# Kernel optimization log

Hardware: AMD Instinct MI355X
Metric: run time of the kernel (lower is better)

Reference implementation:

```python
import jax, jax.numpy as jnp
import numpy as np
from jax import lax

B, T, D = 2, 1024, 2048
HK, HV = 8, 16          # num key heads / num value heads
DK, DV = 128, 128       # head dims
KW = 4                  # conv kernel size
EPS = 1e-6
KEY_DIM = HK * DK
VALUE_DIM = HV * DV
CONV_DIM = 2 * KEY_DIM + VALUE_DIM


def setup_inputs() -> dict:
    key = jax.random.key(0)
    ks = jax.random.split(key, 9)
    w = lambda k, shape, s=0.02: jax.random.normal(k, shape, jnp.float32) * s
    return {
        'hidden_states': jax.random.normal(ks[0], (B, T, D), jnp.float32),
        'W_qkv': w(ks[1], (D, CONV_DIM)),
        'W_z': w(ks[2], (D, VALUE_DIM)),
        'W_b': w(ks[3], (D, HV)),
        'W_a': w(ks[4], (D, HV)),
        'conv_w': w(ks[5], (CONV_DIM, KW), 0.5),
        'dt_bias': jnp.ones((HV,), jnp.float32),
        'A_log': jnp.log(jax.random.uniform(ks[6], (HV,), jnp.float32, 1e-3, 16.0)),
        'norm_weight': jnp.ones((DV,), jnp.float32),
        'W_out': w(ks[7], (VALUE_DIM, D)),
    }


def _causal_conv_silu(x, w):
    # x: [B, C, T], w: [C, K] depthwise causal conv + SiLU (causal_conv1d_fn)
    k = w.shape[1]
    xp = jnp.pad(x, ((0, 0), (0, 0), (k - 1, 0)))
    y = sum(w[:, j][None, :, None] * xp[:, :, j:j + x.shape[2]] for j in range(k))
    return jax.nn.silu(y)


def _l2norm(x):
    return x * lax.rsqrt(jnp.sum(x * x, -1, keepdims=True) + 1e-6)


def reference(hidden_states, W_qkv, W_z, W_b, W_a, conv_w, dt_bias, A_log,
              norm_weight, W_out):
    Bb, Tt, _ = hidden_states.shape
    mixed = hidden_states @ W_qkv                       # [B,T,conv_dim]
    mixed = _causal_conv_silu(mixed.transpose(0, 2, 1), conv_w).transpose(0, 2, 1)
    q, k, v = jnp.split(mixed, [KEY_DIM, 2 * KEY_DIM], axis=-1)
    q = q.reshape(Bb, Tt, HK, DK)
    k = k.reshape(Bb, Tt, HK, DK)
    v = v.reshape(Bb, Tt, HV, DV)
    z = (hidden_states @ W_z).reshape(Bb, Tt, HV, DV)
    beta = jax.nn.sigmoid(hidden_states @ W_b)          # [B,T,HV]
    g = -jnp.exp(A_log) * jax.nn.softplus(hidden_states @ W_a + dt_bias)  # [B,T,HV]

    rep = HV // HK  # GQA: repeat_interleave q,k heads
    q = jnp.repeat(q, rep, axis=2)
    k = jnp.repeat(k, rep, axis=2)
    q = _l2norm(q) * (DK ** -0.5)                       # use_qk_l2norm + scale
    k = _l2norm(k)

    # gated delta-rule recurrence (fp32 state), scanned over time
    qs = q.transpose(1, 0, 2, 3)   # [T,B,HV,DK]
    ks = k.transpose(1, 0, 2, 3)
    vs = v.transpose(1, 0, 2, 3)   # [T,B,HV,DV]
    gs = g.transpose(1, 0, 2)      # [T,B,HV]
    bs = beta.transpose(1, 0, 2)

    def step(S, inp):
        qt, kt, vt, gt, bt = inp
        S = S * jnp.exp(gt)[..., None, None]                          # decay
        v_adj = (vt - jnp.einsum('bhk,bhkv->bhv', kt, S)) * bt[..., None]
        S = S + kt[..., None] * v_adj[..., None, :]                   # rank-1 delta update
        o = jnp.einsum('bhk,bhkv->bhv', qt, S)
        return S, o

    S0 = jnp.zeros((Bb, HV, DK, DV), jnp.float32)
    _, o = lax.scan(step, S0, (qs, ks, vs, gs, bs))
    o = o.transpose(1, 0, 2, 3)                         # [B,T,HV,DV]

    # gated RMSNorm over head_v_dim
    var = jnp.mean(o * o, -1, keepdims=True)
    o = o * lax.rsqrt(var + EPS) * norm_weight
    o = o * jax.nn.silu(z)

    return o.reshape(Bb, Tt, VALUE_DIM) @ W_out         # [B,T,D]
```

## Files before the change

### kernel.cpp

```cpp
#include <hip/hip_runtime.h>
#include <hip/hip_bf16.h>

#define B_ 2
#define T_ 1024
#define D_ 2048
#define HK_ 8
#define HV_ 16
#define DK_ 128
#define DV_ 128
#define KEY_DIM_ 1024
#define VALUE_DIM_ 2048
#define CONV_DIM_ 4096
#define BT_ 2048
#define NCH_ 16
#define CL_ 64

typedef __attribute__((ext_vector_type(8))) short short8;
typedef __attribute__((ext_vector_type(4))) float f32x4;

__device__ __forceinline__ short f2bf(float x) {
  __hip_bfloat16 h = __float2bfloat16(x);
  return *reinterpret_cast<short*>(&h);
}
__device__ __forceinline__ float bf2f(short u) {
  unsigned int x = ((unsigned int)(unsigned short)u) << 16;
  return __int_as_float(x);
}

#define GLOAD_LDS16(g, l)                                             \
  __builtin_amdgcn_global_load_lds(                                   \
      (const __attribute__((address_space(1))) void*)(g),             \
      (__attribute__((address_space(3))) void*)(l), 16, 0, 0)

__global__ void transpose_cast(const float* __restrict__ W, short* __restrict__ WT, int R, int C) {
  __shared__ float tile[32][33];
  int tx = threadIdx.x, ty = threadIdx.y;
  int x = blockIdx.x * 32 + tx;
#pragma unroll
  for (int j = 0; j < 4; ++j) {
    int r = blockIdx.y * 32 + ty + j * 8;
    tile[ty + j * 8][tx] = W[(long)r * C + x];
  }
  __syncthreads();
  int ro = blockIdx.y * 32 + tx;
#pragma unroll
  for (int j = 0; j < 4; ++j) {
    int co = blockIdx.x * 32 + ty + j * 8;
    WT[(long)co * R + ro] = f2bf(tile[tx][ty + j * 8]);
  }
}

__global__ void interleave_ba(const float* __restrict__ Wb, const float* __restrict__ Wa,
                              float* __restrict__ Wba32) {
  int i = blockIdx.x * 256 + threadIdx.x;
  int c = i & 31, k = i >> 5;
  Wba32[i] = (c < 16) ? Wb[k * 16 + c] : Wa[k * 16 + (c - 16)];
}

__global__ __launch_bounds__(256) void gemm128_split(const short* __restrict__ A,
                                                     const short* __restrict__ Bt,
                                                     float* __restrict__ C0,
                                                     float* __restrict__ C1,
                                                     int N0, int N1, int K) {
  __shared__ short As[2][128 * 32];
  __shared__ short Bs[2][128 * 32];
  int m0 = blockIdx.y * 128, n0 = blockIdx.x * 128;
  int tid = threadIdx.x;
  int wave = tid >> 6, lane = tid & 63;
  int wm = (wave >> 1) * 64, wn = (wave & 1) * 64;
  int quad = lane >> 4, l16 = lane & 15;
  f32x4 acc[4][4] = {};

  int ar = tid >> 2;
  int ac = (tid & 3) * 8;
  const short* Ag0 = A + (long)(m0 + ar) * K + ac;
  const short* Ag1 = A + (long)(m0 + 64 + ar) * K + ac;
  const short* Bg0 = Bt + (long)(n0 + ar) * K + ac;
  const short* Bg1 = Bt + (long)(n0 + 64 + ar) * K + ac;
  int NT = K >> 5;

#define STAGE_(t, c)                                  \
  do {                                                \
    GLOAD_LDS16(Ag0 + (t) * 32, As[c] + tid * 8);     \
    GLOAD_LDS16(Ag1 + (t) * 32, As[c] + 64 * 32 + tid * 8); \
    GLOAD_LDS16(Bg0 + (t) * 32, Bs[c] + tid * 8);     \
    GLOAD_LDS16(Bg1 + (t) * 32, Bs[c] + 64 * 32 + tid * 8); \
  } while (0)

  STAGE_(0, 0);
  STAGE_(1, 1);

  for (int t = 0; t < NT; ++t) {
    int c = t & 1;
    if (t + 1 < NT) {
      asm volatile("s_waitcnt vmcnt(4)" ::: "memory");
    } else {
      asm volatile("s_waitcnt vmcnt(0)" ::: "memory");
    }
    __builtin_amdgcn_s_barrier();
    __builtin_amdgcn_sched_barrier(0);

    short8 af[4], bf_[4];
#pragma unroll
    for (int i = 0; i < 4; ++i) af[i] = *(const short8*)(As[c] + (wm + i * 16 + l16) * 32 + quad * 8);
#pragma unroll
    for (int j = 0; j < 4; ++j) bf_[j] = *(const short8*)(Bs[c] + (wn + j * 16 + l16) * 32 + quad * 8);
#pragma unroll
    for (int i = 0; i < 4; ++i)
#pragma unroll
      for (int j = 0; j < 4; ++j)
        acc[i][j] = __builtin_amdgcn_mfma_f32_16x16x32_bf16(af[i], bf_[j], acc[i][j], 0, 0, 0);

    __builtin_amdgcn_sched_barrier(0);
    __builtin_amdgcn_s_barrier();
    if (t + 2 < NT) STAGE_(t + 2, c);
  }

  float* Cw; int ldc, cb;
  if (n0 < N0) { Cw = C0; ldc = N0; cb = n0; }
  else         { Cw = C1; ldc = N1; cb = n0 - N0; }
#pragma unroll
  for (int i = 0; i < 4; ++i)
#pragma unroll
    for (int j = 0; j < 4; ++j)
#pragma unroll
      for (int r = 0; r < 4; ++r) {
        int row = m0 + wm + i * 16 + quad * 4 + r;
        int colx = cb + wn + j * 16 + l16;
        Cw[(long)row * ldc + colx] = acc[i][j][r];
      }
#undef STAGE_
}

__global__ __launch_bounds__(256) void gemm128_ks(const short* __restrict__ A,
                                                  const short* __restrict__ Bt,
                                                  float* __restrict__ Cp,
                                                  int M, int N, int K) {
  __shared__ short As[2][128 * 32];
  __shared__ short Bs[2][128 * 32];
  int m0 = blockIdx.y * 128, n0 = blockIdx.x * 128;
  int kh = K >> 1;
  int kbeg = blockIdx.z * kh;
  int tid = threadIdx.x;
  int wave = tid >> 6, lane = tid & 63;
  int wm = (wave >> 1) * 64, wn = (wave & 1) * 64;
  int quad = lane >> 4, l16 = lane & 15;
  f32x4 acc[4][4] = {};

  int ar = tid >> 2;
  int ac = (tid & 3) * 8;
  const short* Ag0 = A + (long)(m0 + ar) * K + ac + kbeg;
  const short* Ag1 = A + (long)(m0 + 64 + ar) * K + ac + kbeg;
  const short* Bg0 = Bt + (long)(n0 + ar) * K + ac + kbeg;
  const short* Bg1 = Bt + (long)(n0 + 64 + ar) * K + ac + kbeg;
  int NT = kh >> 5;

#define STAGE_(t, c)                                  \
  do {                                                \
    GLOAD_LDS16(Ag0 + (t) * 32, As[c] + tid * 8);     \
    GLOAD_LDS16(Ag1 + (t) * 32, As[c] + 64 * 32 + tid * 8); \
    GLOAD_LDS16(Bg0 + (t) * 32, Bs[c] + tid * 8);     \
    GLOAD_LDS16(Bg1 + (t) * 32, Bs[c] + 64 * 32 + tid * 8); \
  } while (0)

  STAGE_(0, 0);
  STAGE_(1, 1);

  for (int t = 0; t < NT; ++t) {
    int c = t & 1;
    if (t + 1 < NT) {
      asm volatile("s_waitcnt vmcnt(4)" ::: "memory");
    } else {
      asm volatile("s_waitcnt vmcnt(0)" ::: "memory");
    }
    __builtin_amdgcn_s_barrier();
    __builtin_amdgcn_sched_barrier(0);

    short8 af[4], bf_[4];
#pragma unroll
    for (int i = 0; i < 4; ++i) af[i] = *(const short8*)(As[c] + (wm + i * 16 + l16) * 32 + quad * 8);
#pragma unroll
    for (int j = 0; j < 4; ++j) bf_[j] = *(const short8*)(Bs[c] + (wn + j * 16 + l16) * 32 + quad * 8);
#pragma unroll
    for (int i = 0; i < 4; ++i)
#pragma unroll
      for (int j = 0; j < 4; ++j)
        acc[i][j] = __builtin_amdgcn_mfma_f32_16x16x32_bf16(af[i], bf_[j], acc[i][j], 0, 0, 0);

    __builtin_amdgcn_sched_barrier(0);
    __builtin_amdgcn_s_barrier();
    if (t + 2 < NT) STAGE_(t + 2, c);
  }

  float* Cz = Cp + (long)blockIdx.z * M * N;
#pragma unroll
  for (int i = 0; i < 4; ++i)
#pragma unroll
    for (int j = 0; j < 4; ++j)
#pragma unroll
      for (int r = 0; r < 4; ++r) {
        int row = m0 + wm + i * 16 + quad * 4 + r;
        int colx = n0 + wn + j * 16 + l16;
        Cz[(long)row * N + colx] = acc[i][j][r];
      }
#undef STAGE_
}

__global__ void add2(const float* __restrict__ p0, const float* __restrict__ p1,
                     float* __restrict__ out, int n4) {
  int i = blockIdx.x * 256 + threadIdx.x;
  if (i < n4) {
    float4 a = ((const float4*)p0)[i];
    float4 b = ((const float4*)p1)[i];
    float4 o;
    o.x = a.x + b.x; o.y = a.y + b.y; o.z = a.z + b.z; o.w = a.w + b.w;
    ((float4*)out)[i] = o;
  }
}

__global__ __launch_bounds__(256) void small_proj(const float* __restrict__ hidden,
                                                  const float* __restrict__ Wba32,
                                                  const float* __restrict__ dt_bias,
                                                  const float* __restrict__ A_log,
                                                  float* __restrict__ betaT,
                                                  float* __restrict__ gT,
                                                  short* __restrict__ hbf) {
  __shared__ float red[2][32][33];
  int r0 = blockIdx.x * 2;
  int tid = threadIdx.x;
  int cg = tid & 7, s = tid >> 3;
  const f32x4* wp = (const f32x4*)Wba32 + (long)s * 64 * 8 + cg;
  const f32x4* h0 = (const f32x4*)(hidden + (long)r0 * D_ + s * 64);
  const f32x4* h1 = (const f32x4*)(hidden + (long)(r0 + 1) * D_ + s * 64);
  f32x4 a0 = {0.f, 0.f, 0.f, 0.f}, a1 = {0.f, 0.f, 0.f, 0.f};
#pragma unroll
  for (int ii = 0; ii < 16; ++ii) {
    f32x4 ha = h0[ii], hb = h1[ii];
    f32x4 w0 = wp[(ii * 4 + 0) * 8];
    f32x4 w1 = wp[(ii * 4 + 1) * 8];
    f32x4 w2 = wp[(ii * 4 + 2) * 8];
    f32x4 w3 = wp[(ii * 4 + 3) * 8];
    a0 += ha[0] * w0; a1 += hb[0] * w0;
    a0 += ha[1] * w1; a1 += hb[1] * w1;
    a0 += ha[2] * w2; a1 += hb[2] * w2;
    a0 += ha[3] * w3; a1 += hb[3] * w3;
  }
#pragma unroll
  for (int j = 0; j < 4; ++j) {
    red[0][s][cg * 4 + j] = a0[j];
    red[1][s][cg * 4 + j] = a1[j];
  }
  {
    int colb = s * 64 + cg * 8;
    const float* p0 = hidden + (long)r0 * D_ + colb;
    const float* p1 = p0 + D_;
    float4 x0 = *(const float4*)(p0);
    float4 x1 = *(const float4*)(p0 + 4);
    float4 y0 = *(const float4*)(p1);
    float4 y1 = *(const float4*)(p1 + 4);
    short8 o0, o1;
    o0[0] = f2bf(x0.x); o0[1] = f2bf(x0.y); o0[2] = f2bf(x0.z); o0[3] = f2bf(x0.w);
    o0[4] = f2bf(x1.x); o0[5] = f2bf(x1.y); o0[6] = f2bf(x1.z); o0[7] = f2bf(x1.w);
    o1[0] = f2bf(y0.x); o1[1] = f2bf(y0.y); o1[2] = f2bf(y0.z); o1[3] = f2bf(y0.w);
    o1[4] = f2bf(y1.x); o1[5] = f2bf(y1.y); o1[6] = f2bf(y1.z); o1[7] = f2bf(y1.w);
    *(short8*)(hbf + (long)r0 * D_ + colb) = o0;
    *(short8*)(hbf + (long)(r0 + 1) * D_ + colb) = o1;
  }
  __syncthreads();
  if (tid < 64) {
    int row = tid >> 5, c = tid & 31;
    float t0 = 0.f, t1 = 0.f, t2 = 0.f, t3 = 0.f;
#pragma unroll
    for (int ss = 0; ss < 32; ss += 4) {
      t0 += red[row][ss][c];
      t1 += red[row][ss + 1][c];
      t2 += red[row][ss + 2][c];
      t3 += red[row][ss + 3][c];
    }
    float t = (t0 + t1) + (t2 + t3);
    int r = r0 + row;
    if (c < 16) {
      betaT[c * BT_ + r] = 1.f / (1.f + __expf(-t));
    } else {
      int hh = c - 16;
      float y = t + dt_bias[hh];
      float sp = fmaxf(y, 0.f) + log1pf(__expf(-fabsf(y)));
      gT[hh * BT_ + r] = -__expf(A_log[hh]) * sp;
    }
  }
}

__global__ void conv_silu(const float* __restrict__ x, const float* __restrict__ w,
                          float* __restrict__ y) {
  int idx = blockIdx.x * 256 + threadIdx.x;
  int c = idx & (CONV_DIM_ - 1);
  int bt = idx >> 12;
  int t = bt & (T_ - 1);
  float4 wc = *(const float4*)(w + c * 4);
  const float* xp = x + (long)idx;
  float acc = wc.w * xp[0];
  if (t >= 1) acc += wc.z * xp[-CONV_DIM_];
  if (t >= 2) acc += wc.y * xp[-2 * CONV_DIM_];
  if (t >= 3) acc += wc.x * xp[-3 * CONV_DIM_];
  y[idx] = acc * (1.f / (1.f + __expf(-acc)));
}

__global__ __launch_bounds__(64) void qknorm(const float* __restrict__ qkv,
                                             short* __restrict__ qb, short* __restrict__ kb) {
  int bi = blockIdx.x;
  int which = bi & 1;
  int h = (bi >> 1) & 7;
  int bt = bi >> 4;
  int lane = threadIdx.x;
  const float* src = qkv + (long)bt * CONV_DIM_ + which * KEY_DIM_ + h * DK_;
  float2 v = *(const float2*)(src + lane * 2);
  float ss = v.x * v.x + v.y * v.y;
#pragma unroll
  for (int m = 32; m; m >>= 1) ss += __shfl_xor(ss, m, 64);
  float scale = rsqrtf(ss + 1e-6f);
  if (which == 0) scale *= 0.08838834764831845f;
  short* dst = (which ? kb : qb) + ((long)bt * HK_ + h) * DK_;
  short2 o; o.x = f2bf(v.x * scale); o.y = f2bf(v.y * scale);
  ((short2*)dst)[lane] = o;
}

__global__ __launch_bounds__(256, 2) void chunk_phase1(
    const short* __restrict__ qbf, const short* __restrict__ kbf,
    const float* __restrict__ qkv, const float* __restrict__ gT,
    const float* __restrict__ bT,
    short* __restrict__ Pm, short* __restrict__ GQ, short* __restrict__ KtT,
    short* __restrict__ Wneg, float* __restrict__ Ut, float* __restrict__ Gammac) {
  __shared__ float Al[64 * 64];
  __shared__ float Gs[64], Gam[64], Dd[64], Bet[64], BG[64];

  int ci = blockIdx.x;
  int c = ci & 15, hv = (ci >> 4) & 15, b = ci >> 8;
  int hk = hv >> 1;
  int t0 = c * CL_;
  int tid = threadIdx.x;
  int wave = tid >> 6, lane = tid & 63, quad = lane >> 4, l16 = lane & 15;

  if (tid < 64) {
    float g = gT[(hv * B_ + b) * T_ + t0 + tid];
    float x = g;
#pragma unroll
    for (int off = 1; off < 64; off <<= 1) {
      float y = __shfl_up(x, off, 64);
      if (tid >= off) x += y;
    }
    Gs[tid] = x;
    float gm = __expf(x);
    Gam[tid] = gm;
    float Gtot = __shfl(x, 63, 64);
    Dd[tid] = __expf(Gtot - x);
    float bb = bT[(hv * B_ + b) * T_ + t0 + tid];
    Bet[tid] = bb;
    BG[tid] = bb * gm;
    if (tid == 63) Gammac[ci] = __expf(x);
  }
  __syncthreads();

  const long kbase = ((long)(b * T_ + t0) * HK_ + hk) * DK_;
  const int kstride = HK_ * DK_;

  int half = tid >> 7;
  int col = tid & 127;
  float u[64];
  {
    const float* vcol = qkv + (long)(b * T_ + t0) * CONV_DIM_ + 2 * KEY_DIM_ + hv * DV_ + col;
    const short* kcol = kbf + kbase + col;
    if (half == 0) {
#pragma unroll
      for (int r = 0; r < 64; ++r) u[r] = vcol[(long)r * CONV_DIM_];
    } else {
#pragma unroll
      for (int r = 0; r < 64; ++r) u[r] = bf2f(kcol[(long)r * kstride]);
    }
  }

  {
    f32x4 acc[4] = {};
#pragma unroll
    for (int kk = 0; kk < 4; ++kk) {
      short8 afr = *(const short8*)(kbf + kbase + (long)(16 * wave + l16) * kstride + kk * 32 + quad * 8);
#pragma unroll
      for (int j = 0; j < 4; ++j) {
        short8 bfr = *(const short8*)(kbf + kbase + (long)(16 * j + l16) * kstride + kk * 32 + quad * 8);
        acc[j] = __builtin_amdgcn_mfma_f32_16x16x32_bf16(afr, bfr, acc[j], 0, 0, 0);
      }
    }
#pragma unroll
    for (int j = 0; j < 4; ++j)
#pragma unroll
      for (int r = 0; r < 4; ++r) {
        int row = 16 * wave + quad * 4 + r, colx = 16 * j + l16;
        float v = 0.f;
        if (row > colx) v = Bet[row] * __expf(Gs[row] - Gs[colx]) * acc[j][r];
        Al[row * 64 + colx] = v;
      }
  }
  {
    f32x4 acc[4] = {};
#pragma unroll
    for (int kk = 0; kk < 4; ++kk) {
      short8 afr = *(const short8*)(qbf + kbase + (long)(16 * wave + l16) * kstride + kk * 32 + quad * 8);
#pragma unroll
      for (int j = 0; j < 4; ++j) {
        short8 bfr = *(const short8*)(kbf + kbase + (long)(16 * j + l16) * kstride + kk * 32 + quad * 8);
        acc[j] = __builtin_amdgcn_mfma_f32_16x16x32_bf16(afr, bfr, acc[j], 0, 0, 0);
      }
    }
#pragma unroll
    for (int j = 0; j < 4; ++j)
#pragma unroll
      for (int r = 0; r < 4; ++r) {
        int row = 16 * wave + quad * 4 + r, colx = 16 * j + l16;
        float v = 0.f;
        if (row >= colx) v = __expf(Gs[row] - Gs[colx]) * acc[j][r];
        Pm[(long)ci * 4096 + row * 64 + colx] = f2bf(v);
      }
  }
  for (int s = wave; s < 64; s += 4) {
    float gm = Gam[s];
    short2 qv = *(const short2*)(qbf + kbase + (long)s * kstride + lane * 2);
    short2 o;
    o.x = f2bf(bf2f(qv.x) * gm);
    o.y = f2bf(bf2f(qv.y) * gm);
    *(short2*)(GQ + (long)ci * 8192 + s * 128 + lane * 2) = o;
  }
  for (int d = wave; d < 128; d += 4) {
    float kv = bf2f(kbf[kbase + (long)lane * kstride + d]);
    KtT[(long)ci * 8192 + d * 64 + lane] = f2bf(kv * Dd[lane]);
  }
  __syncthreads();

  if (half == 0) {
#pragma unroll
    for (int r = 0; r < 64; ++r) u[r] *= Bet[r];
  } else {
#pragma unroll
    for (int r = 0; r < 64; ++r) u[r] *= BG[r];
  }
#pragma unroll
  for (int s = 1; s < 64; ++s) {
    const float* Ar = Al + s * 64;
    float acc = 0.f;
#pragma unroll
    for (int r4 = 0; r4 + 4 <= s; r4 += 4) {
      float4 a = *(const float4*)(Ar + r4);
      acc += (a.x * u[r4] + a.y * u[r4 + 1]) + (a.z * u[r4 + 2] + a.w * u[r4 + 3]);
    }
#pragma unroll
    for (int r = (s / 4) * 4; r < s; ++r) acc += Ar[r] * u[r];
    u[s] -= acc;
  }
  if (half == 0) {
    float* up = Ut + (long)ci * 8192 + col;
#pragma unroll
    for (int s = 0; s < 64; ++s) up[s * 128] = u[s];
  } else {
    short* wp = Wneg + (long)ci * 8192 + col;
#pragma unroll
    for (int s = 0; s < 64; ++s) wp[s * 128] = f2bf(-u[s]);
  }
}

__global__ __launch_bounds__(256) void chunk_phase2(
    const short* __restrict__ Wneg, const float* __restrict__ Ut,
    const short* __restrict__ KtT, const float* __restrict__ Gammac,
    short* __restrict__ UTg, short* __restrict__ ScTg) {
  __shared__ short SLT[16 * 136];
  __shared__ short ULT[16 * 72];
  int bi = blockIdx.x >> 3;
  int n0 = (blockIdx.x & 7) * 16;
  int tid = threadIdx.x, wave = tid >> 6, lane = tid & 63, quad = lane >> 4, l16 = lane & 15;
  f32x4 S2[2] = {};

  long ci0 = (long)bi * NCH_;
  short8 Wr[4]; f32x4 Ur; short8 Kr[2][2];
  {
    long ci = ci0;
#pragma unroll
    for (int kk = 0; kk < 4; ++kk)
      Wr[kk] = *(const short8*)(Wneg + ci * 8192 + (16 * wave + l16) * 128 + kk * 32 + quad * 8);
    const float* up = Ut + ci * 8192 + (16 * wave + quad * 4) * 128 + n0 + l16;
#pragma unroll
    for (int r = 0; r < 4; ++r) Ur[r] = up[r * 128];
#pragma unroll
    for (int kk = 0; kk < 2; ++kk)
#pragma unroll
      for (int i = 0; i < 2; ++i)
        Kr[kk][i] = *(const short8*)(KtT + ci * 8192 + (32 * wave + 16 * i + l16) * 64 + kk * 32 + quad * 8);
  }

  for (int ch = 0; ch < NCH_; ++ch) {
    long ci = ci0 + ch;
#pragma unroll
    for (int i = 0; i < 2; ++i) {
      int m0 = 32 * wave + 16 * i + quad * 4;
      short4 p;
      p.x = f2bf(S2[i][0]); p.y = f2bf(S2[i][1]);
      p.z = f2bf(S2[i][2]); p.w = f2bf(S2[i][3]);
      *(short4*)(SLT + l16 * 136 + m0) = p;
      *(short4*)(ScTg + ci * 16384 + (n0 + l16) * 128 + m0) = p;
    }
    short8 Wn[4]; f32x4 Un; short8 Kn[2][2];
    if (ch + 1 < NCH_) {
      long cj = ci + 1;
#pragma unroll
      for (int kk = 0; kk < 4; ++kk)
        Wn[kk] = *(const short8*)(Wneg + cj * 8192 + (16 * wave + l16) * 128 + kk * 32 + quad * 8);
      const float* up = Ut + cj * 8192 + (16 * wave + quad * 4) * 128 + n0 + l16;
#pragma unroll
      for (int r = 0; r < 4; ++r) Un[r] = up[r * 128];
#pragma unroll
      for (int kk = 0; kk < 2; ++kk)
#pragma unroll
        for (int i = 0; i < 2; ++i)
          Kn[kk][i] = *(const short8*)(KtT + cj * 8192 + (32 * wave + 16 * i + l16) * 64 + kk * 32 + quad * 8);
    }
    __syncthreads();
    f32x4 Ua = Ur;
#pragma unroll
    for (int kk = 0; kk < 4; ++kk) {
      short8 bfv = *(const short8*)(SLT + l16 * 136 + kk * 32 + quad * 8);
      Ua = __builtin_amdgcn_mfma_f32_16x16x32_bf16(Wr[kk], bfv, Ua, 0, 0, 0);
    }
    {
      int s0 = 16 * wave + quad * 4;
      short4 p;
      p.x = f2bf(Ua[0]); p.y = f2bf(Ua[1]); p.z = f2bf(Ua[2]); p.w = f2bf(Ua[3]);
      *(short4*)(ULT + l16 * 72 + s0) = p;
      *(short4*)(UTg + ci * 8192 + (n0 + l16) * 64 + s0) = p;
    }
    __syncthreads();
    float gc = Gammac[ci];
#pragma unroll
    for (int i = 0; i < 2; ++i)
#pragma unroll
      for (int r = 0; r < 4; ++r) S2[i][r] *= gc;
#pragma unroll
    for (int kk = 0; kk < 2; ++kk) {
      short8 bfv = *(const short8*)(ULT + l16 * 72 + kk * 32 + quad * 8);
#pragma unroll
      for (int i = 0; i < 2; ++i)
        S2[i] = __builtin_amdgcn_mfma_f32_16x16x32_bf16(Kr[kk][i], bfv, S2[i], 0, 0, 0);
    }
    __syncthreads();
    if (ch + 1 < NCH_) {
#pragma unroll
      for (int kk = 0; kk < 4; ++kk) Wr[kk] = Wn[kk];
      Ur = Un;
#pragma unroll
      for (int kk = 0; kk < 2; ++kk)
#pragma unroll
        for (int i = 0; i < 2; ++i) Kr[kk][i] = Kn[kk][i];
    }
  }
}

__global__ __launch_bounds__(256) void chunk_phase3(
    const short* __restrict__ GQ, const short* __restrict__ ScTg,
    const short* __restrict__ Pm, const short* __restrict__ UTg,
    const float* __restrict__ zbuf, const float* __restrict__ nw,
    short* __restrict__ obf) {
  int ci = blockIdx.x;
  int c = ci & 15, hv = (ci >> 4) & 15, b = ci >> 8;
  int t0 = c * CL_;
  int tid = threadIdx.x, wave = tid >> 6, lane = tid & 63, quad = lane >> 4, l16 = lane & 15;
  f32x4 acc[8] = {};
#pragma unroll
  for (int kk = 0; kk < 4; ++kk) {
    short8 af = *(const short8*)(GQ + (long)ci * 8192 + (16 * wave + l16) * 128 + kk * 32 + quad * 8);
#pragma unroll
    for (int j = 0; j < 8; ++j) {
      short8 bfv = *(const short8*)(ScTg + (long)ci * 16384 + (16 * j + l16) * 128 + kk * 32 + quad * 8);
      acc[j] = __builtin_amdgcn_mfma_f32_16x16x32_bf16(af, bfv, acc[j], 0, 0, 0);
    }
  }
#pragma unroll
  for (int kk = 0; kk < 2; ++kk) {
    short8 af = *(const short8*)(Pm + (long)ci * 4096 + (16 * wave + l16) * 64 + kk * 32 + quad * 8);
#pragma unroll
    for (int j = 0; j < 8; ++j) {
      short8 bfv = *(const short8*)(UTg + (long)ci * 8192 + (16 * j + l16) * 64 + kk * 32 + quad * 8);
      acc[j] = __builtin_amdgcn_mfma_f32_16x16x32_bf16(af, bfv, acc[j], 0, 0, 0);
    }
  }
#pragma unroll
  for (int r = 0; r < 4; ++r) {
    float ss = 0.f;
#pragma unroll
    for (int j = 0; j < 8; ++j) ss += acc[j][r] * acc[j][r];
    ss += __shfl_xor(ss, 1, 64);
    ss += __shfl_xor(ss, 2, 64);
    ss += __shfl_xor(ss, 4, 64);
    ss += __shfl_xor(ss, 8, 64);
    float scale = rsqrtf(ss * (1.f / 128.f) + 1e-6f);
    int t = t0 + 16 * wave + quad * 4 + r;
    long base = (long)(b * T_ + t) * VALUE_DIM_ + hv * DV_;
#pragma unroll
    for (int j = 0; j < 8; ++j) {
      int n = 16 * j + l16;
      float zv = zbuf[base + n];
      float sz = zv * (1.f / (1.f + __expf(-zv)));
      obf[base + n] = f2bf(acc[j][r] * scale * nw[n] * sz);
    }
  }
}

extern "C" void kernel_launch(void* const* d_in, const int* in_sizes, int n_in,
                              void* d_out, int out_size, void* d_ws, size_t ws_size,
                              hipStream_t stream) {
  const float* hidden  = (const float*)d_in[0];
  const float* W_qkv   = (const float*)d_in[1];
  const float* W_z     = (const float*)d_in[2];
  const float* W_b     = (const float*)d_in[3];
  const float* W_a     = (const float*)d_in[4];
  const float* conv_w  = (const float*)d_in[5];
  const float* dt_bias = (const float*)d_in[6];
  const float* A_log   = (const float*)d_in[7];
  const float* norm_w  = (const float*)d_in[8];
  const float* W_out   = (const float*)d_in[9];
  float* out = (float*)d_out;

  char* ws = (char*)d_ws;
  size_t off = 0;
  auto alloc = [&](size_t bytes) {
    void* p = ws + off;
    off += (bytes + 255) & ~(size_t)255;
    return p;
  };
  short* hidden_bf = (short*)alloc((size_t)BT_ * D_ * 2);
  short* WcatT     = (short*)alloc((size_t)(CONV_DIM_ + VALUE_DIM_) * D_ * 2);
  short* WoutT     = (short*)alloc((size_t)D_ * VALUE_DIM_ * 2);
  float* mixed     = (float*)alloc((size_t)BT_ * CONV_DIM_ * 4);
  float* qkv       = (float*)alloc((size_t)BT_ * CONV_DIM_ * 4);
  float* zbuf      = (float*)alloc((size_t)BT_ * VALUE_DIM_ * 4);
  short* qbf       = (short*)alloc((size_t)BT_ * KEY_DIM_ * 2);
  short* kbf       = (short*)alloc((size_t)BT_ * KEY_DIM_ * 2);
  float* betab     = (float*)alloc((size_t)BT_ * HV_ * 4);
  float* gb        = (float*)alloc((size_t)BT_ * HV_ * 4);
  float* Wba32     = (float*)alloc((size_t)D_ * 32 * 4);
  short* Wneg      = (short*)alloc((size_t)512 * 8192 * 2);
  float* Ut32      = (float*)alloc((size_t)512 * 8192 * 4);
  short* KtT       = (short*)alloc((size_t)512 * 8192 * 2);
  short* UTg       = (short*)alloc((size_t)512 * 8192 * 2);
  short* ScTg      = (short*)alloc((size_t)512 * 16384 * 2);
  float* Gammac    = (float*)alloc((size_t)512 * 4);
  short* Pm   = (short*)(mixed + (size_t)BT_ * VALUE_DIM_);
  short* GQ   = Pm + (size_t)512 * 4096;
  short* obf  = hidden_bf;
  float* Cpart = qkv;

  dim3 tb32(32, 8);
  transpose_cast<<<dim3(CONV_DIM_ / 32, D_ / 32), tb32, 0, stream>>>(W_qkv, WcatT, D_, CONV_DIM_);
  transpose_cast<<<dim3(VALUE_DIM_ / 32, D_ / 32), tb32, 0, stream>>>(W_z, WcatT + (size_t)CONV_DIM_ * D_, D_, VALUE_DIM_);
  transpose_cast<<<dim3(D_ / 32, VALUE_DIM_ / 32), tb32, 0, stream>>>(W_out, WoutT, VALUE_DIM_, D_);
  interleave_ba<<<32 * D_ / 256, 256, 0, stream>>>(W_b, W_a, Wba32);

  small_proj<<<BT_ / 2, 256, 0, stream>>>(hidden, Wba32, dt_bias, A_log, betab, gb, hidden_bf);

  gemm128_split<<<dim3((CONV_DIM_ + VALUE_DIM_) / 128, BT_ / 128), 256, 0, stream>>>(
      hidden_bf, WcatT, mixed, zbuf, CONV_DIM_, VALUE_DIM_, D_);
  conv_silu<<<BT_ * CONV_DIM_ / 256, 256, 0, stream>>>(mixed, conv_w, qkv);
  qknorm<<<BT_ * HK_ * 2, 64, 0, stream>>>(qkv, qbf, kbf);

  chunk_phase1<<<512, 256, 0, stream>>>(qbf, kbf, qkv, gb, betab, Pm, GQ, KtT, Wneg, Ut32, Gammac);
  chunk_phase2<<<256, 256, 0, stream>>>(Wneg, Ut32, KtT, Gammac, UTg, ScTg);
  chunk_phase3<<<512, 256, 0, stream>>>(GQ, ScTg, Pm, UTg, zbuf, norm_w, obf);

  gemm128_ks<<<dim3(D_ / 128, BT_ / 128, 2), 256, 0, stream>>>(obf, WoutT, Cpart, BT_, D_, VALUE_DIM_);
  add2<<<(BT_ * D_ / 4 + 255) / 256, 256, 0, stream>>>(Cpart, Cpart + (size_t)BT_ * D_, out, BT_ * D_ / 4);
}
```

Baseline: 376.0 us.

## Rewrite input projection GEMM as 256x256 tile, 8-wave pipelined kernel

Replaces the 128x128, 4-wave input-projection GEMM with a 256x256 tile, 8-wave kernel using BK=64. It uses XOR-swizzled LDS layout, finer-grained staggered global-to-LDS loads interleaved with MFMA phases, and s_setprio around MFMA bursts. The aim is more data reuse per loaded byte and better overlap of loads with matrix math. The grid shrinks to 24x8=192 blocks, which may leave some CUs idle on a large GPU, and the 128 KB LDS buffer limits occupancy.

```diff
diff --git a/kernel.cpp b/kernel.cpp
--- a/kernel.cpp
+++ b/kernel.cpp
@@ -57,79 +57,236 @@
   Wba32[i] = (c < 16) ? Wb[k * 16 + c] : Wa[k * 16 + (c - 16)];
 }
 
-__global__ __launch_bounds__(256) void gemm128_split(const short* __restrict__ A,
+__global__ __launch_bounds__(512) void gemm256_split(const short* __restrict__ A,
                                                      const short* __restrict__ Bt,
                                                      float* __restrict__ C0,
                                                      float* __restrict__ C1,
                                                      int N0, int N1, int K) {
-  __shared__ short As[2][128 * 32];
-  __shared__ short Bs[2][128 * 32];
-  int m0 = blockIdx.y * 128, n0 = blockIdx.x * 128;
-  int tid = threadIdx.x;
-  int wave = tid >> 6, lane = tid & 63;
-  int wm = (wave >> 1) * 64, wn = (wave & 1) * 64;
-  int quad = lane >> 4, l16 = lane & 15;
-  f32x4 acc[4][4] = {};
-
-  int ar = tid >> 2;
-  int ac = (tid & 3) * 8;
-  const short* Ag0 = A + (long)(m0 + ar) * K + ac;
-  const short* Ag1 = A + (long)(m0 + 64 + ar) * K + ac;
-  const short* Bg0 = Bt + (long)(n0 + ar) * K + ac;
-  const short* Bg1 = Bt + (long)(n0 + 64 + ar) * K + ac;
-  int NT = K >> 5;
-
-#define STAGE_(t, c)                                  \
-  do {                                                \
-    GLOAD_LDS16(Ag0 + (t) * 32, As[c] + tid * 8);     \
-    GLOAD_LDS16(Ag1 + (t) * 32, As[c] + 64 * 32 + tid * 8); \
-    GLOAD_LDS16(Bg0 + (t) * 32, Bs[c] + tid * 8);     \
-    GLOAD_LDS16(Bg1 + (t) * 32, Bs[c] + 64 * 32 + tid * 8); \
-  } while (0)
-
-  STAGE_(0, 0);
-  STAGE_(1, 1);
-
-  for (int t = 0; t < NT; ++t) {
-    int c = t & 1;
-    if (t + 1 < NT) {
-      asm volatile("s_waitcnt vmcnt(4)" ::: "memory");
-    } else {
-      asm volatile("s_waitcnt vmcnt(0)" ::: "memory");
-    }
-    __builtin_amdgcn_s_barrier();
-    __builtin_amdgcn_sched_barrier(0);
-
-    short8 af[4], bf_[4];
-#pragma unroll
-    for (int i = 0; i < 4; ++i) af[i] = *(const short8*)(As[c] + (wm + i * 16 + l16) * 32 + quad * 8);
-#pragma unroll
-    for (int j = 0; j < 4; ++j) bf_[j] = *(const short8*)(Bs[c] + (wn + j * 16 + l16) * 32 + quad * 8);
-#pragma unroll
-    for (int i = 0; i < 4; ++i)
-#pragma unroll
-      for (int j = 0; j < 4; ++j)
-        acc[i][j] = __builtin_amdgcn_mfma_f32_16x16x32_bf16(af[i], bf_[j], acc[i][j], 0, 0, 0);
-
-    __builtin_amdgcn_sched_barrier(0);
-    __builtin_amdgcn_s_barrier();
-    if (t + 2 < NT) STAGE_(t + 2, c);
+  __shared__ short lds[65536];
+  const int tid = threadIdx.x;
+  const int lane = tid & 63, wid = tid >> 6;
+  const int quad = lane >> 4, l16 = lane & 15;
+  const int wm = (wid >> 2) * 128, wn = (wid & 3) * 64;
+  const int m0 = blockIdx.y * 256, n0 = blockIdx.x * 256;
+
+  const int r8 = tid >> 3, t8 = (tid & 7) * 8;
+  const int csw = t8 ^ ((r8 & 7) << 3);
+  const int rB = (r8 & 31) + ((r8 >> 5) << 6);
+  const int cswr = (quad ^ (l16 & 7)) << 3;
+  const int NT = K >> 6, NIT = NT >> 1;
+
+  f32x4 acc[8][4] = {};
+  short8 a[4][2], bl[2][2], bh[2][2];
+
+#define SGA(p, kt, rb)                                                        \
+  GLOAD_LDS16(A + (long)(m0 + (rb) + r8) * K + (kt) * 64 + csw,               \
+              lds + (p) * 32768 + ((rb) + r8) * 64 + t8)
+#define SGB(p, kt, rb)                                                        \
+  GLOAD_LDS16(Bt + (long)(n0 + (rb) + rB) * K + (kt) * 64 + csw,              \
+              lds + (p) * 32768 + 16384 + ((rb) + rB) * 64 + t8)
+#define UA0(p, kt) do { SGA(p, kt, 0);  SGA(p, kt, 128); } while (0)
+#define UA2(p, kt) do { SGA(p, kt, 64); SGA(p, kt, 192); } while (0)
+#define UB1(p, kt) do { SGB(p, kt, 0);  SGB(p, kt, 128); } while (0)
+#define UB3(p, kt) do { SGB(p, kt, 32); SGB(p, kt, 160); } while (0)
+#define RDA(p, r, kk) (*(const short8*)(lds + (p) * 32768 + (r) * 64 + (cswr ^ ((kk) << 5))))
+#define RDB(p, r, kk) (*(const short8*)(lds + (p) * 32768 + 16384 + (r) * 64 + (cswr ^ ((kk) << 5))))
+#define MFMA_(d, x, y) d = __builtin_amdgcn_mfma_f32_16x16x32_bf16(x, y, d, 0, 0, 0)
+#define BAR_() do { __builtin_amdgcn_s_barrier(); __builtin_amdgcn_sched_barrier(0); } while (0)
+#define PRIO_ON_() __builtin_amdgcn_s_setprio(1)
+#define PRIO_OFF_() do { __builtin_amdgcn_s_setprio(0); __builtin_amdgcn_sched_barrier(0); } while (0)
+
+  UA0(0, 0); UB1(0, 0); UA2(0, 0); UB3(0, 0);
+  UA0(1, 1); UB1(1, 1); UA2(1, 1);
+  asm volatile("s_waitcnt vmcnt(6)" ::: "memory");
+  BAR_();
+
+#pragma unroll 1
+  for (int i = 0; i < NIT; ++i) {
+    const int tb = 2 * i + 1, tc = 2 * i + 2, td = 2 * i + 3;
+    const bool more = (i + 1 < NIT);
+
+#pragma unroll
+    for (int mi = 0; mi < 4; ++mi) {
+      a[mi][0] = RDA(0, wm + mi * 16 + l16, 0);
+      a[mi][1] = RDA(0, wm + mi * 16 + l16, 1);
+    }
+#pragma unroll
+    for (int ni = 0; ni < 2; ++ni) {
+      bl[ni][0] = RDB(0, wn + ni * 16 + l16, 0);
+      bl[ni][1] = RDB(0, wn + ni * 16 + l16, 1);
+    }
+    UB3(1, tb);
+    BAR_();
+    PRIO_ON_();
+#pragma unroll
+    for (int mi = 0; mi < 4; ++mi)
+#pragma unroll
+      for (int ni = 0; ni < 2; ++ni) {
+        MFMA_(acc[mi][ni], a[mi][0], bl[ni][0]);
+        MFMA_(acc[mi][ni], a[mi][1], bl[ni][1]);
+      }
+    PRIO_OFF_();
+    __builtin_amdgcn_s_barrier();
+
+    __builtin_amdgcn_sched_barrier(0);
+#pragma unroll
+    for (int ni = 0; ni < 2; ++ni) {
+      bh[ni][0] = RDB(0, wn + 32 + ni * 16 + l16, 0);
+      bh[ni][1] = RDB(0, wn + 32 + ni * 16 + l16, 1);
+    }
+    if (more) UA0(0, tc);
+    BAR_();
+    PRIO_ON_();
+#pragma unroll
+    for (int mi = 0; mi < 4; ++mi)
+#pragma unroll
+      for (int ni = 0; ni < 2; ++ni) {
+        MFMA_(acc[mi][2 + ni], a[mi][0], bh[ni][0]);
+        MFMA_(acc[mi][2 + ni], a[mi][1], bh[ni][1]);
+      }
+    PRIO_OFF_();
+    __builtin_amdgcn_s_barrier();
+
+    __builtin_amdgcn_sched_barrier(0);
+#pragma unroll
+    for (int mi = 0; mi < 4; ++mi) {
+      a[mi][0] = RDA(0, wm + 64 + mi * 16 + l16, 0);
+      a[mi][1] = RDA(0, wm + 64 + mi * 16 + l16, 1);
+    }
+    if (more) UB1(0, tc);
+    BAR_();
+    PRIO_ON_();
+#pragma unroll
+    for (int mi = 0; mi < 4; ++mi)
+#pragma unroll
+      for (int ni = 0; ni < 2; ++ni) {
+        MFMA_(acc[4 + mi][2 + ni], a[mi][0], bh[ni][0]);
+        MFMA_(acc[4 + mi][2 + ni], a[mi][1], bh[ni][1]);
+      }
+    PRIO_OFF_();
+    __builtin_amdgcn_s_barrier();
+
+    __builtin_amdgcn_sched_barrier(0);
+    if (more) UA2(0, tc);
+    BAR_();
+    PRIO_ON_();
+#pragma unroll
+    for (int mi = 0; mi < 4; ++mi)
+#pragma unroll
+      for (int ni = 0; ni < 2; ++ni) {
+        MFMA_(acc[4 + mi][ni], a[mi][0], bl[ni][0]);
+        MFMA_(acc[4 + mi][ni], a[mi][1], bl[ni][1]);
+      }
+    PRIO_OFF_();
+    if (more) { asm volatile("s_waitcnt vmcnt(6)" ::: "memory"); }
+    else      { asm volatile("s_waitcnt vmcnt(0)" ::: "memory"); }
+    __builtin_amdgcn_s_barrier();
+
+    __builtin_amdgcn_sched_barrier(0);
+#pragma unroll
+    for (int mi = 0; mi < 4; ++mi) {
+      a[mi][0] = RDA(1, wm + mi * 16 + l16, 0);
+      a[mi][1] = RDA(1, wm + mi * 16 + l16, 1);
+    }
+#pragma unroll
+    for (int ni = 0; ni < 2; ++ni) {
+      bl[ni][0] = RDB(1, wn + ni * 16 + l16, 0);
+      bl[ni][1] = RDB(1, wn + ni * 16 + l16, 1);
+    }
+    if (more) UB3(0, tc);
+    BAR_();
+    PRIO_ON_();
+#pragma unroll
+    for (int mi = 0; mi < 4; ++mi)
+#pragma unroll
+      for (int ni = 0; ni < 2; ++ni) {
+        MFMA_(acc[mi][ni], a[mi][0], bl[ni][0]);
+        MFMA_(acc[mi][ni], a[mi][1], bl[ni][1]);
+      }
+    PRIO_OFF_();
+    __builtin_amdgcn_s_barrier();
+
+    __builtin_amdgcn_sched_barrier(0);
+#pragma unroll
+    for (int ni = 0; ni < 2; ++ni) {
+      bh[ni][0] = RDB(1, wn + 32 + ni * 16 + l16, 0);
+      bh[ni][1] = RDB(1, wn + 32 + ni * 16 + l16, 1);
+    }
+    if (more) UA0(1, td);
+    BAR_();
+    PRIO_ON_();
+#pragma unroll
+    for (int mi = 0; mi < 4; ++mi)
+#pragma unroll
+      for (int ni = 0; ni < 2; ++ni) {
+        MFMA_(acc[mi][2 + ni], a[mi][0], bh[ni][0]);
+        MFMA_(acc[mi][2 + ni], a[mi][1], bh[ni][1]);
+      }
+    PRIO_OFF_();
+    __builtin_amdgcn_s_barrier();
+
+    __builtin_amdgcn_sched_barrier(0);
+#pragma unroll
+    for (int mi = 0; mi < 4; ++mi) {
+      a[mi][0] = RDA(1, wm + 64 + mi * 16 + l16, 0);
+      a[mi][1] = RDA(1, wm + 64 + mi * 16 + l16, 1);
+    }
+    if (more) UB1(1, td);
+    BAR_();
+    PRIO_ON_();
+#pragma unroll
+    for (int mi = 0; mi < 4; ++mi)
+#pragma unroll
+      for (int ni = 0; ni < 2; ++ni) {
+        MFMA_(acc[4 + mi][2 + ni], a[mi][0], bh[ni][0]);
+        MFMA_(acc[4 + mi][2 + ni], a[mi][1], bh[ni][1]);
+      }
+    PRIO_OFF_();
+    __builtin_amdgcn_s_barrier();
+
+    __builtin_amdgcn_sched_barrier(0);
+    if (more) UA2(1, td);
+    BAR_();
+    PRIO_ON_();
+#pragma unroll
+    for (int mi = 0; mi < 4; ++mi)
+#pragma unroll
+      for (int ni = 0; ni < 2; ++ni) {
+        MFMA_(acc[4 + mi][ni], a[mi][0], bl[ni][0]);
+        MFMA_(acc[4 + mi][ni], a[mi][1], bl[ni][1]);
+      }
+    PRIO_OFF_();
+    if (more) { asm volatile("s_waitcnt vmcnt(6)" ::: "memory"); }
+    else      { asm volatile("s_waitcnt vmcnt(0)" ::: "memory"); }
+    __builtin_amdgcn_s_barrier();
+    __builtin_amdgcn_sched_barrier(0);
   }
 
   float* Cw; int ldc, cb;
   if (n0 < N0) { Cw = C0; ldc = N0; cb = n0; }
   else         { Cw = C1; ldc = N1; cb = n0 - N0; }
 #pragma unroll
-  for (int i = 0; i < 4; ++i)
-#pragma unroll
-    for (int j = 0; j < 4; ++j)
+  for (int mi = 0; mi < 8; ++mi)
+#pragma unroll
+    for (int ni = 0; ni < 4; ++ni)
 #pragma unroll
       for (int r = 0; r < 4; ++r) {
-        int row = m0 + wm + i * 16 + quad * 4 + r;
-        int colx = cb + wn + j * 16 + l16;
-        Cw[(long)row * ldc + colx] = acc[i][j][r];
-      }
-#undef STAGE_
+        int row = m0 + wm + mi * 16 + quad * 4 + r;
+        int col = cb + wn + ni * 16 + l16;
+        Cw[(long)row * ldc + col] = acc[mi][ni][r];
+      }
+#undef SGA
+#undef SGB
+#undef UA0
+#undef UA2
+#undef UB1
+#undef UB3
+#undef RDA
+#undef RDB
+#undef MFMA_
+#undef BAR_
+#undef PRIO_ON_
+#undef PRIO_OFF_
 }
 
 __global__ __launch_bounds__(256) void gemm128_ks(const short* __restrict__ A,
@@ -661,7 +818,7 @@
 
   small_proj<<<BT_ / 2, 256, 0, stream>>>(hidden, Wba32, dt_bias, A_log, betab, gb, hidden_bf);
 
-  gemm128_split<<<dim3((CONV_DIM_ + VALUE_DIM_) / 128, BT_ / 128), 256, 0, stream>>>(
+  gemm256_split<<<dim3((CONV_DIM_ + VALUE_DIM_) / 256, BT_ / 256), 512, 0, stream>>>(
       hidden_bf, WcatT, mixed, zbuf, CONV_DIM_, VALUE_DIM_, D_);
   conv_silu<<<BT_ * CONV_DIM_ / 256, 256, 0, stream>>>(mixed, conv_w, qkv);
   qknorm<<<BT_ * HK_ * 2, 64, 0, stream>>>(qkv, qbf, kbf);
```

Result: no change. 379.2 us (+0.9%).
